# Kernel optimization log

Hardware: AMD Instinct MI355X
Metric: run time of the kernel (lower is better)

The kernel has to match this reference:

```python
import jax, jax.numpy as jnp
import numpy as np

N = 50000       # spatial graph nodes (brain mesh vertices)
K = 1024        # spectral components / spectral-graph nodes
E = 200000      # spatial edges
E_SPEC = 16384  # spectral-graph edges
IN_CH = 3       # vertex coordinates
H = 64          # all hidden_channels forced to 64 by shared LayerNorm(64)
NEG = 0.01      # leaky_relu negative slope (torch default)
EPS = 1e-5      # layernorm eps (torch default)


def _ln(x, g, b):
    mu = jnp.mean(x, -1, keepdims=True)
    var = jnp.mean((x - mu) ** 2, -1, keepdims=True)
    return (x - mu) * jax.lax.rsqrt(var + EPS) * g + b


def _lrelu(x):
    return jnp.where(x >= 0, x, NEG * x)


def _edge_conv(x, ei, W, b, n):
    # PyG EdgeConv: max_j nn(cat([x_i, x_j - x_i])), aggregated at target i = ei[1]
    src, dst = ei[0], ei[1]
    xi = x[dst]
    msg = jnp.concatenate([xi, x[src] - xi], -1) @ W.T + b  # [E, out]
    out = jax.ops.segment_max(msg, dst, num_segments=n)
    return jnp.where(jnp.isfinite(out), out, 0.0)  # zeros for isolated nodes


def _forward(x, u, e, edge_index, spec_edge, p):
    ln = lambda t: _ln(t, p["ln_g"], p["ln_b"])
    s0 = ln(_lrelu(ln(_lrelu(e @ p["se1_w"].T + p["se1_b"])) @ p["se2_w"].T + p["se2_b"]))
    x0 = ln(_lrelu(ln(_lrelu(x @ p["sp1_w"].T + p["sp1_b"])) @ p["sp2_w"].T + p["sp2_b"]))
    s1 = ln(_lrelu(_edge_conv(s0, spec_edge, p["c1_w"], p["c1_b"], K)))
    x1 = ln(_lrelu(_edge_conv(x0, edge_index, p["c5_w"], p["c5_b"], N)))
    s1 = jnp.concatenate([s1, u.T @ x0], 1)   # [K, 128]
    x1 = jnp.concatenate([x1, u @ s0], 1)     # [N, 128]
    s2 = jnp.concatenate([s0, s1], 1)         # [K, 192]
    x2 = jnp.concatenate([x0, x1], 1)         # [N, 192]
    s2 = ln(_lrelu(_edge_conv(s2, spec_edge, p["c2_w"], p["c2_b"], K)))
    x2 = ln(_lrelu(_edge_conv(x2, edge_index, p["c6_w"], p["c6_b"], N)))
    s2 = jnp.concatenate([s2, u.T @ x1], 1)   # [K, 192]
    x2 = jnp.concatenate([x2, u @ s1], 1)     # [N, 192]
    s3 = jnp.concatenate([s0, s1, s2], 1)     # [K, 384]
    x3 = jnp.concatenate([x0, x1, x2], 1)     # [N, 384]
    s3 = ln(_lrelu(_edge_conv(s3, spec_edge, p["c3_w"], p["c3_b"], K)))
    x3 = ln(_lrelu(_edge_conv(x3, edge_index, p["c7_w"], p["c7_b"], N)))
    s3 = jnp.concatenate([s3, u.T @ x2], 1)   # [K, 256]
    x3 = jnp.concatenate([x3, u @ s2], 1)     # [N, 256]
    x4 = jnp.concatenate([x0, x1, x2, x3], 1)  # [N, 640]
    x4 = ln(_lrelu(_edge_conv(x4, edge_index, p["c8_w"], p["c8_b"], N)))
    x4 = jnp.concatenate([x4, u @ s3], 1)      # [N, 320]
    x4 = jnp.concatenate([x0, x1, x2, x3, x4], 1)  # [N, 960]
    out = ln(_lrelu(x4 @ p["d1_w"].T + p["d1_b"]))  # dropout = identity (eval)
    return out @ p["d2_w"].T + p["d2_b"]            # [N, 32]


def setup_inputs() -> dict:
    key = jax.random.key(0)
    ks = iter(jax.random.split(key, 24))
    def w(shape):
        return jax.random.normal(next(ks), shape, jnp.float32) * 0.05
    inp = {
        "x": jax.random.normal(next(ks), (N, IN_CH), jnp.float32),
        "u": jax.random.normal(next(ks), (N, K), jnp.float32) * 0.03,
        "e": jax.random.normal(next(ks), (K, 1), jnp.float32),
        "edge_index": jax.random.randint(next(ks), (2, E), 0, N, jnp.int32),
        "spec_edge": jax.random.randint(next(ks), (2, E_SPEC), 0, K, jnp.int32),
    }
    shapes = {
        "se1_w": (H, 1), "se2_w": (H, H), "sp1_w": (H, IN_CH), "sp2_w": (H, H),
        "c1_w": (H, 2 * 64), "c2_w": (H, 2 * 192), "c3_w": (H, 2 * 384),
        "c5_w": (H, 2 * 64), "c6_w": (H, 2 * 192), "c7_w": (H, 2 * 384),
        "c8_w": (H, 2 * 640), "d1_w": (H, 960), "d2_w": (32, H),
    }
    for name, s in shapes.items():
        inp[name] = w(s)
        inp[name.replace("_w", "_b")] = jnp.zeros((s[0],), jnp.float32)
    inp["ln_g"] = jnp.ones((H,), jnp.float32)
    inp["ln_b"] = jnp.zeros((H,), jnp.float32)
    return inp


def reference(x, u, e, edge_index, spec_edge,
              se1_w, se1_b, se2_w, se2_b, sp1_w, sp1_b, sp2_w, sp2_b,
              c1_w, c1_b, c2_w, c2_b, c3_w, c3_b,
              c5_w, c5_b, c6_w, c6_b, c7_w, c7_b, c8_w, c8_b,
              d1_w, d1_b, d2_w, d2_b, ln_g, ln_b):
    p = dict(locals())
    for k in ("x", "u", "e", "edge_index", "spec_edge"):
        p.pop(k)
    return _forward(x, u, e, edge_index, spec_edge, p)
```

## Files before the change

kernel.cpp:

```cpp
#include <hip/hip_runtime.h>
#include <hip/hip_bf16.h>


typedef __attribute__((ext_vector_type(8))) short bf16x8;
typedef __attribute__((ext_vector_type(4))) float f32x4;

#define DEVFN __device__ __forceinline__

constexpr int NN   = 50000;
constexpr int KKn  = 1024;
constexpr int EEe  = 200000;
constexpr int ESn  = 16384;
constexpr int NPAD = 50016;
constexpr int NKB  = 1563;

DEVFN short f2bf(float v) {
  unsigned b = __float_as_uint(v);
  unsigned r = (b + 0x7FFFu + ((b >> 16) & 1u)) >> 16;
  return (short)r;
}
DEVFN float lrelu(float v) { return v >= 0.f ? v : 0.01f * v; }
DEVFN float wsum64(float v) {
#pragma unroll
  for (int m = 32; m; m >>= 1) v += __shfl_xor(v, m, 64);
  return v;
}
DEVFN float ln64(float v, float g, float b) {
  float mu  = wsum64(v) * 0.015625f;
  float d   = v - mu;
  float var = wsum64(d * d) * 0.015625f;
  return d * rsqrtf(var + 1e-5f) * g + b;
}

__global__ void transpose_u_k(const float* __restrict__ u, short* __restrict__ ub,
                              short* __restrict__ ut) {
  __shared__ float tile[32][33];
  int kt = blockIdx.x, ntile = blockIdx.y;
  int tx = threadIdx.x, ty = threadIdx.y;
#pragma unroll
  for (int r = 0; r < 32; r += 8) {
    int n = ntile * 32 + ty + r;
    int k = kt * 32 + tx;
    float v = 0.f;
    if (n < NN) {
      v = u[(long)n * 1024 + k];
      ub[(long)n * 1024 + k] = f2bf(v);
    }
    tile[ty + r][tx] = v;
  }
  __syncthreads();
#pragma unroll
  for (int r = 0; r < 32; r += 8) {
    int k = kt * 32 + ty + r;
    int n = ntile * 32 + tx;
    ut[(long)k * NPAD + n] = f2bf(tile[tx][ty + r]);
  }
}

__global__ void pack_b_k(const short* __restrict__ src, int lds_, int coloff,
                         int Kred, int kb_total, int C, short* __restrict__ dst) {
  long t = (long)blockIdx.x * 256 + threadIdx.x;
  long total = (long)kb_total * 32 * C;
  if (t >= total) return;
  int k = (int)(t / C);
  int c = (int)(t - (long)k * C);
  short v = (k < Kred) ? src[(long)k * lds_ + coloff + c] : (short)0;
  long pa = (long)(k >> 5) * (32 * C) + ((c >> 4) << 9) + (((k >> 3) & 3) << 7)
          + ((c & 15) << 3) + (k & 7);
  dst[pa] = v;
}

__global__ void pack_wcat_k(const float* __restrict__ W, int F, short* __restrict__ dst) {
  int t = blockIdx.x * 256 + threadIdx.x;
  if (t >= F * 128) return;
  int f = t >> 7, c = t & 127;
  float v = (c < 64) ? (W[c * 2 * F + f] - W[c * 2 * F + F + f])
                     : W[(c - 64) * 2 * F + F + f];
  long pa = (long)(f >> 5) * (32 * 128) + ((c >> 4) << 9) + (((f >> 3) & 3) << 7)
          + ((c & 15) << 3) + (f & 7);
  dst[pa] = f2bf(v);
}

__global__ void pack_d1t_k(const float* __restrict__ W, short* __restrict__ dst) {
  int t = blockIdx.x * 256 + threadIdx.x;
  if (t >= 960 * 64) return;
  int f = t >> 6, c = t & 63;
  float v = W[c * 960 + f];
  long pa = (long)(f >> 5) * (32 * 64) + ((c >> 4) << 9) + (((f >> 3) & 3) << 7)
          + ((c & 15) << 3) + (f & 7);
  dst[pa] = f2bf(v);
}

template <int NT, int EPI>
__launch_bounds__(256)
__global__ void gemm_k(const short* __restrict__ A, int lda,
                       const short* __restrict__ Bp,
                       void* __restrict__ outp, int ldo, int coloff,
                       int M, int kb_total, int kb_chunk) {
  constexpr int C = NT * 16;
  __shared__ short bsm[32 * C];
  const int tid  = threadIdx.x;
  const int lane = tid & 63;
  const int wave = tid >> 6;
  const int mtile = blockIdx.x;
  int kb0 = blockIdx.y * kb_chunk;
  int kb1 = min(kb0 + kb_chunk, kb_total);
  const int row  = mtile * 64 + wave * 16 + (lane & 15);
  const long arow = (long)min(row, M - 1) * lda + ((lane >> 4) * 8);
  f32x4 acc[NT];
#pragma unroll
  for (int t = 0; t < NT; ++t) acc[t] = (f32x4){0.f, 0.f, 0.f, 0.f};

  for (int kb = kb0; kb < kb1; ++kb) {
    const short* bsrc = Bp + (long)kb * (32 * C);
    bf16x8 tmp[NT / 4];
#pragma unroll
    for (int r = 0; r < NT / 4; ++r)
      tmp[r] = *(const bf16x8*)(bsrc + (r * 256 + tid) * 8);
    bf16x8 a = *(const bf16x8*)(A + arow + (long)kb * 32);
    __syncthreads();
#pragma unroll
    for (int r = 0; r < NT / 4; ++r)
      *(bf16x8*)(bsm + (r * 256 + tid) * 8) = tmp[r];
    __syncthreads();
#pragma unroll
    for (int t = 0; t < NT; ++t) {
      bf16x8 b = *(const bf16x8*)(bsm + t * 512 + lane * 8);
      acc[t] = __builtin_amdgcn_mfma_f32_16x16x32_bf16(a, b, acc[t], 0, 0, 0);
    }
  }
  const int cb = lane & 15;
  const int rbase = mtile * 64 + wave * 16 + ((lane >> 4) * 4);
#pragma unroll
  for (int t = 0; t < NT; ++t) {
#pragma unroll
    for (int r = 0; r < 4; ++r) {
      int rr = rbase + r;
      if (rr < M) {
        long idx = (long)rr * ldo + coloff + t * 16 + cb;
        if constexpr (EPI == 0)      ((float*)outp)[idx] = acc[t][r];
        else if constexpr (EPI == 1) ((short*)outp)[idx] = f2bf(acc[t][r]);
        else                          atomicAdd((float*)outp + idx, acc[t][r]);
      }
    }
  }
}

__global__ void mlp_spec_k(const float* __restrict__ e, const float* __restrict__ w1,
                           const float* __restrict__ b1, const float* __restrict__ w2,
                           const float* __restrict__ b2, const float* __restrict__ g,
                           const float* __restrict__ bl, short* __restrict__ feat, int ldf) {
  int t = blockIdx.x * 256 + threadIdx.x;
  int i = t >> 6, lane = t & 63;
  if (i >= KKn) return;
  float ev = e[i];
  float h = lrelu(ev * w1[lane] + b1[lane]);
  h = ln64(h, g[lane], bl[lane]);
  float a = b2[lane];
  for (int j = 0; j < 64; ++j) a += __shfl(h, j, 64) * w2[lane * 64 + j];
  a = lrelu(a); a = ln64(a, g[lane], bl[lane]);
  feat[(long)i * ldf + lane] = f2bf(a);
}

__global__ void mlp_sp_k(const float* __restrict__ x, const float* __restrict__ w1,
                         const float* __restrict__ b1, const float* __restrict__ w2,
                         const float* __restrict__ b2, const float* __restrict__ g,
                         const float* __restrict__ bl, short* __restrict__ feat, int ldf) {
  int t = blockIdx.x * 256 + threadIdx.x;
  int i = t >> 6, lane = t & 63;
  if (i >= NN) return;
  float x0 = x[i * 3 + 0], x1 = x[i * 3 + 1], x2 = x[i * 3 + 2];
  float h = x0 * w1[lane * 3 + 0] + x1 * w1[lane * 3 + 1] + x2 * w1[lane * 3 + 2] + b1[lane];
  h = lrelu(h); h = ln64(h, g[lane], bl[lane]);
  float a = b2[lane];
  for (int j = 0; j < 64; ++j) a += __shfl(h, j, 64) * w2[lane * 64 + j];
  a = lrelu(a); a = ln64(a, g[lane], bl[lane]);
  feat[(long)i * ldf + lane] = f2bf(a);
}

__global__ void edge_max_k(const int* __restrict__ ei, int E, const float* __restrict__ PQ,
                           unsigned* __restrict__ mc) {
  int t = blockIdx.x * 256 + threadIdx.x;
  int e = t >> 6, lane = t & 63;
  if (e >= E) return;
  int src = ei[e], dst = ei[E + e];
  float v = PQ[(long)src * 128 + 64 + lane];
  unsigned b = __float_as_uint(v);
  unsigned code = b ^ ((unsigned)(((int)b) >> 31) | 0x80000000u);
  atomicMax(mc + (long)dst * 64 + lane, code);
}

__global__ void segfin_k(const float* __restrict__ PQ, const unsigned* __restrict__ mc,
                         const float* __restrict__ bias, const float* __restrict__ g,
                         const float* __restrict__ bl, short* __restrict__ feat,
                         int ldf, int coloff, int n) {
  int t = blockIdx.x * 256 + threadIdx.x;
  int i = t >> 6, lane = t & 63;
  if (i >= n) return;
  unsigned code = mc[(long)i * 64 + lane];
  float v = 0.f;
  if (code) {
    unsigned ub = code ^ ((code & 0x80000000u) ? 0x80000000u : 0xFFFFFFFFu);
    v = PQ[(long)i * 128 + lane] + bias[lane] + __uint_as_float(ub);
  }
  v = lrelu(v);
  v = ln64(v, g[lane], bl[lane]);
  feat[(long)i * ldf + coloff + lane] = f2bf(v);
}

__global__ void zconv_k(const float* __restrict__ Z, short* __restrict__ feat,
                        int C, int coloff) {
  int t = blockIdx.x * 256 + threadIdx.x;
  if (t >= KKn * C) return;
  int k = t / C, c = t - k * C;
  feat[(long)k * 640 + coloff + c] = f2bf(Z[t]);
}

__global__ void final_k(const float* __restrict__ H, const float* __restrict__ d1b,
                        const float* __restrict__ d2w, const float* __restrict__ d2b,
                        const float* __restrict__ g, const float* __restrict__ bl,
                        float* __restrict__ out) {
  int t = blockIdx.x * 256 + threadIdx.x;
  int i = t >> 6, lane = t & 63;
  if (i >= NN) return;
  float v = H[(long)i * 64 + lane] + d1b[lane];
  v = lrelu(v);
  v = ln64(v, g[lane], bl[lane]);
  int c = lane & 31;
  int jbase = (lane >> 5) * 32;
  float acc = 0.f;
#pragma unroll
  for (int j = 0; j < 32; ++j)
    acc += __shfl(v, jbase + j, 64) * d2w[c * 64 + jbase + j];
  acc += __shfl_down(acc, 32, 64);
  if (lane < 32) out[(long)i * 32 + c] = acc + d2b[c];
}

extern "C" void kernel_launch(void* const* d_in, const int* in_sizes, int n_in,
                              void* d_out, int out_size, void* d_ws, size_t ws_size,
                              hipStream_t stream) {
  const float* x    = (const float*)d_in[0];
  const float* u    = (const float*)d_in[1];
  const float* e    = (const float*)d_in[2];
  const int*   ei   = (const int*)d_in[3];
  const int*   sei  = (const int*)d_in[4];
  const float* se1w = (const float*)d_in[5];  const float* se1b = (const float*)d_in[6];
  const float* se2w = (const float*)d_in[7];  const float* se2b = (const float*)d_in[8];
  const float* sp1w = (const float*)d_in[9];  const float* sp1b = (const float*)d_in[10];
  const float* sp2w = (const float*)d_in[11]; const float* sp2b = (const float*)d_in[12];
  const float* c1w = (const float*)d_in[13];  const float* c1b = (const float*)d_in[14];
  const float* c2w = (const float*)d_in[15];  const float* c2b = (const float*)d_in[16];
  const float* c3w = (const float*)d_in[17];  const float* c3b = (const float*)d_in[18];
  const float* c5w = (const float*)d_in[19];  const float* c5b = (const float*)d_in[20];
  const float* c6w = (const float*)d_in[21];  const float* c6b = (const float*)d_in[22];
  const float* c7w = (const float*)d_in[23];  const float* c7b = (const float*)d_in[24];
  const float* c8w = (const float*)d_in[25];  const float* c8b = (const float*)d_in[26];
  const float* d1w = (const float*)d_in[27];  const float* d1b = (const float*)d_in[28];
  const float* d2w = (const float*)d_in[29];  const float* d2b = (const float*)d_in[30];
  const float* lng = (const float*)d_in[31];  const float* lnb = (const float*)d_in[32];

  char* ws = (char*)d_ws;
  size_t off = 0;
  auto alloc = [&](size_t bytes) -> void* {
    void* p = ws + off;
    off = (off + bytes + 255) & ~(size_t)255;
    return p;
  };
  short* u_bf  = (short*)alloc((size_t)NN * 1024 * 2);
  short* uT    = (short*)alloc((size_t)KKn * NPAD * 2);
  short* xfeat = (short*)alloc((size_t)NN * 960 * 2);
  short* sfeat = (short*)alloc((size_t)KKn * 640 * 2);
  float* PQx   = (float*)alloc((size_t)NN * 128 * 4);
  float* PQs   = (float*)alloc((size_t)KKn * 128 * 4);
  char* zbase = ws + off;
  unsigned* mx  = (unsigned*)alloc((size_t)NN * 64 * 4);
  unsigned* ms  = (unsigned*)alloc((size_t)KKn * 64 * 4);
  float* Zs0 = (float*)alloc((size_t)KKn * 64 * 4);
  float* Zs1 = (float*)alloc((size_t)KKn * 128 * 4);
  float* Zs2 = (float*)alloc((size_t)KKn * 192 * 4);
  size_t zbytes = (size_t)((ws + off) - zbase);
  short* ypack = (short*)alloc((size_t)KKn * 256 * 2);
  short* zpack = (short*)alloc((size_t)NPAD * 192 * 2);
  short* wc1 = (short*)alloc(64  * 128 * 2);
  short* wc2 = (short*)alloc(192 * 128 * 2);
  short* wc3 = (short*)alloc(384 * 128 * 2);
  short* wc5 = (short*)alloc(64  * 128 * 2);
  short* wc6 = (short*)alloc(192 * 128 * 2);
  short* wc7 = (short*)alloc(384 * 128 * 2);
  short* wc8 = (short*)alloc(640 * 128 * 2);
  short* d1tp = (short*)alloc(960 * 64 * 2);
  float* Hbuf = PQx;

  const size_t MXB = (size_t)NN * 64 * 4;
  const size_t MSB = (size_t)KKn * 64 * 4;

  hipMemsetAsync(zbase, 0, zbytes, stream);
  transpose_u_k<<<dim3(32, NKB), dim3(32, 8), 0, stream>>>(u, u_bf, uT);
  pack_wcat_k<<<32,  256, 0, stream>>>(c1w, 64,  wc1);
  pack_wcat_k<<<96,  256, 0, stream>>>(c2w, 192, wc2);
  pack_wcat_k<<<192, 256, 0, stream>>>(c3w, 384, wc3);
  pack_wcat_k<<<32,  256, 0, stream>>>(c5w, 64,  wc5);
  pack_wcat_k<<<96,  256, 0, stream>>>(c6w, 192, wc6);
  pack_wcat_k<<<192, 256, 0, stream>>>(c7w, 384, wc7);
  pack_wcat_k<<<320, 256, 0, stream>>>(c8w, 640, wc8);
  pack_d1t_k<<<240, 256, 0, stream>>>(d1w, d1tp);
  mlp_spec_k<<<256,   256, 0, stream>>>(e, se1w, se1b, se2w, se2b, lng, lnb, sfeat, 640);
  mlp_sp_k<<<12500,   256, 0, stream>>>(x, sp1w, sp1b, sp2w, sp2b, lng, lnb, xfeat, 960);

  const int GX = (NN + 63) / 64;

  gemm_k<8, 0><<<dim3(GX, 1), 256, 0, stream>>>(xfeat, 960, wc5, PQx, 128, 0, NN, 2, 2);
  gemm_k<8, 0><<<dim3(16, 1), 256, 0, stream>>>(sfeat, 640, wc1, PQs, 128, 0, KKn, 2, 2);
  edge_max_k<<<50000, 256, 0, stream>>>(ei, EEe, PQx, mx);
  edge_max_k<<<4096,  256, 0, stream>>>(sei, ESn, PQs, ms);
  segfin_k<<<12500, 256, 0, stream>>>(PQx, mx, c5b, lng, lnb, xfeat, 960, 64, NN);
  segfin_k<<<256,   256, 0, stream>>>(PQs, ms, c1b, lng, lnb, sfeat, 640, 64, KKn);
  pack_b_k<<<256, 256, 0, stream>>>(sfeat, 640, 0, KKn, 32, 64, ypack);
  gemm_k<4, 1><<<dim3(GX, 1), 256, 0, stream>>>(u_bf, 1024, ypack, xfeat, 960, 128, NN, 32, 32);
  pack_b_k<<<12504, 256, 0, stream>>>(xfeat, 960, 0, NN, NKB, 64, zpack);
  gemm_k<4, 2><<<dim3(16, 16), 256, 0, stream>>>(uT, NPAD, zpack, Zs0, 64, 0, KKn, NKB, 98);
  zconv_k<<<256, 256, 0, stream>>>(Zs0, sfeat, 64, 128);

  hipMemsetAsync(mx, 0, MXB, stream);
  hipMemsetAsync(ms, 0, MSB, stream);
  gemm_k<8, 0><<<dim3(GX, 1), 256, 0, stream>>>(xfeat, 960, wc6, PQx, 128, 0, NN, 6, 6);
  gemm_k<8, 0><<<dim3(16, 1), 256, 0, stream>>>(sfeat, 640, wc2, PQs, 128, 0, KKn, 6, 6);
  edge_max_k<<<50000, 256, 0, stream>>>(ei, EEe, PQx, mx);
  edge_max_k<<<4096,  256, 0, stream>>>(sei, ESn, PQs, ms);
  segfin_k<<<12500, 256, 0, stream>>>(PQx, mx, c6b, lng, lnb, xfeat, 960, 192, NN);
  segfin_k<<<256,   256, 0, stream>>>(PQs, ms, c2b, lng, lnb, sfeat, 640, 192, KKn);
  pack_b_k<<<512, 256, 0, stream>>>(sfeat, 640, 64, KKn, 32, 128, ypack);
  gemm_k<8, 1><<<dim3(GX, 1), 256, 0, stream>>>(u_bf, 1024, ypack, xfeat, 960, 256, NN, 32, 32);
  pack_b_k<<<25008, 256, 0, stream>>>(xfeat, 960, 64, NN, NKB, 128, zpack);
  gemm_k<8, 2><<<dim3(16, 16), 256, 0, stream>>>(uT, NPAD, zpack, Zs1, 128, 0, KKn, NKB, 98);
  zconv_k<<<512, 256, 0, stream>>>(Zs1, sfeat, 128, 256);

  hipMemsetAsync(mx, 0, MXB, stream);
  hipMemsetAsync(ms, 0, MSB, stream);
  gemm_k<8, 0><<<dim3(GX, 1), 256, 0, stream>>>(xfeat, 960, wc7, PQx, 128, 0, NN, 12, 12);
  gemm_k<8, 0><<<dim3(16, 1), 256, 0, stream>>>(sfeat, 640, wc3, PQs, 128, 0, KKn, 12, 12);
  edge_max_k<<<50000, 256, 0, stream>>>(ei, EEe, PQx, mx);
  edge_max_k<<<4096,  256, 0, stream>>>(sei, ESn, PQs, ms);
  segfin_k<<<12500, 256, 0, stream>>>(PQx, mx, c7b, lng, lnb, xfeat, 960, 384, NN);
  segfin_k<<<256,   256, 0, stream>>>(PQs, ms, c3b, lng, lnb, sfeat, 640, 384, KKn);
  pack_b_k<<<768, 256, 0, stream>>>(sfeat, 640, 192, KKn, 32, 192, ypack);
  gemm_k<12, 1><<<dim3(GX, 1), 256, 0, stream>>>(u_bf, 1024, ypack, xfeat, 960, 448, NN, 32, 32);
  pack_b_k<<<37512, 256, 0, stream>>>(xfeat, 960, 192, NN, NKB, 192, zpack);
  gemm_k<12, 2><<<dim3(16, 16), 256, 0, stream>>>(uT, NPAD, zpack, Zs2, 192, 0, KKn, NKB, 98);
  zconv_k<<<768, 256, 0, stream>>>(Zs2, sfeat, 192, 448);

  hipMemsetAsync(mx, 0, MXB, stream);
  gemm_k<8, 0><<<dim3(GX, 1), 256, 0, stream>>>(xfeat, 960, wc8, PQx, 128, 0, NN, 20, 20);
  edge_max_k<<<50000, 256, 0, stream>>>(ei, EEe, PQx, mx);
  segfin_k<<<12500, 256, 0, stream>>>(PQx, mx, c8b, lng, lnb, xfeat, 960, 640, NN);
  pack_b_k<<<1024, 256, 0, stream>>>(sfeat, 640, 384, KKn, 32, 256, ypack);
  gemm_k<16, 1><<<dim3(GX, 1), 256, 0, stream>>>(u_bf, 1024, ypack, xfeat, 960, 704, NN, 32, 32);

  gemm_k<4, 0><<<dim3(GX, 1), 256, 0, stream>>>(xfeat, 960, d1tp, Hbuf, 64, 0, NN, 30, 30);
  final_k<<<12500, 256, 0, stream>>>(Hbuf, d1b, d2w, d2b, lng, lnb, (float*)d_out);

  (void)in_sizes; (void)n_in; (void)out_size; (void)ws_size;
}
```

Baseline: 1.430 ms.

## Merge paired spatial/spectral launches, drop LDS staging in GEMM, widen transpose

Paired spatial and spectral GEMM, edge-max and segment-finalize launches are merged into single kernels that branch on block index, cutting launch count and letting the small spectral work fill gaps. The GEMM no longer stages B through shared memory with two barriers per k-step; each lane reads its pre-packed B fragment straight from global memory, relying on cache reuse across waves. The u transpose now uses 64x64 bf16 tiles with vectorized float4 loads and ushort4 stores, and the padding grows to 50048/1564 to fit the larger tile. Direct global B loads could add cache traffic in place of LDS reads, and the narrow ushort4 transposed stores and LDS bank pattern may not be ideal.

```diff
diff --git a/kernel.cpp b/kernel.cpp
--- a/kernel.cpp
+++ b/kernel.cpp
@@ -11,8 +11,8 @@
 constexpr int KKn  = 1024;
 constexpr int EEe  = 200000;
 constexpr int ESn  = 16384;
-constexpr int NPAD = 50016;
-constexpr int NKB  = 1563;
+constexpr int NPAD = 50048;
+constexpr int NKB  = 1564;
 
 DEVFN short f2bf(float v) {
   unsigned b = __float_as_uint(v);
@@ -34,26 +34,34 @@
 
 __global__ void transpose_u_k(const float* __restrict__ u, short* __restrict__ ub,
                               short* __restrict__ ut) {
-  __shared__ float tile[32][33];
-  int kt = blockIdx.x, ntile = blockIdx.y;
-  int tx = threadIdx.x, ty = threadIdx.y;
-#pragma unroll
-  for (int r = 0; r < 32; r += 8) {
-    int n = ntile * 32 + ty + r;
-    int k = kt * 32 + tx;
-    float v = 0.f;
-    if (n < NN) {
-      v = u[(long)n * 1024 + k];
-      ub[(long)n * 1024 + k] = f2bf(v);
-    }
-    tile[ty + r][tx] = v;
+  __shared__ unsigned short tile[64][66];
+  const int kt  = blockIdx.x;
+  const int nt0 = blockIdx.y;
+  const int tx = threadIdx.x & 15, ty = threadIdx.x >> 4;
+  const int kbase = kt * 64;
+#pragma unroll
+  for (int r = 0; r < 64; r += 16) {
+    int nl = ty + r;
+    int n  = nt0 * 64 + nl;
+    float4 v = {0.f, 0.f, 0.f, 0.f};
+    if (n < NN) v = *(const float4*)(u + (long)n * 1024 + kbase + tx * 4);
+    ushort4 w;
+    w.x = (unsigned short)f2bf(v.x); w.y = (unsigned short)f2bf(v.y);
+    w.z = (unsigned short)f2bf(v.z); w.w = (unsigned short)f2bf(v.w);
+    if (n < NN) *(ushort4*)(ub + (long)n * 1024 + kbase + tx * 4) = w;
+    tile[nl][tx * 4 + 0] = w.x; tile[nl][tx * 4 + 1] = w.y;
+    tile[nl][tx * 4 + 2] = w.z; tile[nl][tx * 4 + 3] = w.w;
   }
   __syncthreads();
 #pragma unroll
-  for (int r = 0; r < 32; r += 8) {
-    int k = kt * 32 + ty + r;
-    int n = ntile * 32 + tx;
-    ut[(long)k * NPAD + n] = f2bf(tile[tx][ty + r]);
+  for (int r = 0; r < 64; r += 16) {
+    int kl = ty + r;
+    int k  = kbase + kl;
+    int n0 = nt0 * 64 + tx * 4;
+    ushort4 w;
+    w.x = tile[tx * 4 + 0][kl]; w.y = tile[tx * 4 + 1][kl];
+    w.z = tile[tx * 4 + 2][kl]; w.w = tile[tx * 4 + 3][kl];
+    *(ushort4*)(ut + (long)k * NPAD + n0) = w;
   }
 }
 
@@ -92,40 +100,25 @@
 }
 
 template <int NT, int EPI>
-__launch_bounds__(256)
-__global__ void gemm_k(const short* __restrict__ A, int lda,
-                       const short* __restrict__ Bp,
-                       void* __restrict__ outp, int ldo, int coloff,
-                       int M, int kb_total, int kb_chunk) {
-  constexpr int C = NT * 16;
-  __shared__ short bsm[32 * C];
-  const int tid  = threadIdx.x;
-  const int lane = tid & 63;
-  const int wave = tid >> 6;
-  const int mtile = blockIdx.x;
-  int kb0 = blockIdx.y * kb_chunk;
-  int kb1 = min(kb0 + kb_chunk, kb_total);
+DEVFN void gemm_body(const short* __restrict__ A, int lda,
+                     const short* __restrict__ Bp,
+                     void* __restrict__ outp, int ldo, int coloff,
+                     int M, int mtile, int kb0, int kb1) {
+  const int lane = threadIdx.x & 63;
+  const int wave = threadIdx.x >> 6;
   const int row  = mtile * 64 + wave * 16 + (lane & 15);
   const long arow = (long)min(row, M - 1) * lda + ((lane >> 4) * 8);
+  const short* bl = Bp + lane * 8;
   f32x4 acc[NT];
 #pragma unroll
   for (int t = 0; t < NT; ++t) acc[t] = (f32x4){0.f, 0.f, 0.f, 0.f};
 
   for (int kb = kb0; kb < kb1; ++kb) {
-    const short* bsrc = Bp + (long)kb * (32 * C);
-    bf16x8 tmp[NT / 4];
-#pragma unroll
-    for (int r = 0; r < NT / 4; ++r)
-      tmp[r] = *(const bf16x8*)(bsrc + (r * 256 + tid) * 8);
     bf16x8 a = *(const bf16x8*)(A + arow + (long)kb * 32);
-    __syncthreads();
-#pragma unroll
-    for (int r = 0; r < NT / 4; ++r)
-      *(bf16x8*)(bsm + (r * 256 + tid) * 8) = tmp[r];
-    __syncthreads();
+    const short* bsrc = bl + (long)kb * (NT * 512);
 #pragma unroll
     for (int t = 0; t < NT; ++t) {
-      bf16x8 b = *(const bf16x8*)(bsm + t * 512 + lane * 8);
+      bf16x8 b = *(const bf16x8*)(bsrc + t * 512);
       acc[t] = __builtin_amdgcn_mfma_f32_16x16x32_bf16(a, b, acc[t], 0, 0, 0);
     }
   }
@@ -146,6 +139,29 @@
   }
 }
 
+template <int NT, int EPI>
+__launch_bounds__(256)
+__global__ void gemm_k(const short* __restrict__ A, int lda,
+                       const short* __restrict__ Bp,
+                       void* __restrict__ outp, int ldo, int coloff,
+                       int M, int kb_total, int kb_chunk) {
+  int kb0 = blockIdx.y * kb_chunk;
+  int kb1 = min(kb0 + kb_chunk, kb_total);
+  gemm_body<NT, EPI>(A, lda, Bp, outp, ldo, coloff, M, blockIdx.x, kb0, kb1);
+}
+
+template <int NT>
+__launch_bounds__(256)
+__global__ void gemmx2_k(const short* __restrict__ A0, int lda0,
+                         const short* __restrict__ B0, float* out0, int M0, int GX0,
+                         const short* __restrict__ A1, int lda1,
+                         const short* __restrict__ B1, float* out1, int M1,
+                         int kb_total) {
+  int b = blockIdx.x;
+  if (b < GX0) gemm_body<NT, 0>(A0, lda0, B0, out0, 128, 0, M0, b, 0, kb_total);
+  else         gemm_body<NT, 0>(A1, lda1, B1, out1, 128, 0, M1, b - GX0, 0, kb_total);
+}
+
 __global__ void mlp_spec_k(const float* __restrict__ e, const float* __restrict__ w1,
                            const float* __restrict__ b1, const float* __restrict__ w2,
                            const float* __restrict__ b2, const float* __restrict__ g,
@@ -178,10 +194,8 @@
   feat[(long)i * ldf + lane] = f2bf(a);
 }
 
-__global__ void edge_max_k(const int* __restrict__ ei, int E, const float* __restrict__ PQ,
-                           unsigned* __restrict__ mc) {
-  int t = blockIdx.x * 256 + threadIdx.x;
-  int e = t >> 6, lane = t & 63;
+DEVFN void edge_max_body(const int* __restrict__ ei, int E, const float* __restrict__ PQ,
+                         unsigned* __restrict__ mc, int e, int lane) {
   if (e >= E) return;
   int src = ei[e], dst = ei[E + e];
   float v = PQ[(long)src * 128 + 64 + lane];
@@ -190,12 +204,25 @@
   atomicMax(mc + (long)dst * 64 + lane, code);
 }
 
-__global__ void segfin_k(const float* __restrict__ PQ, const unsigned* __restrict__ mc,
-                         const float* __restrict__ bias, const float* __restrict__ g,
-                         const float* __restrict__ bl, short* __restrict__ feat,
-                         int ldf, int coloff, int n) {
-  int t = blockIdx.x * 256 + threadIdx.x;
-  int i = t >> 6, lane = t & 63;
+__global__ void edge_max_k(const int* __restrict__ ei, int E, const float* __restrict__ PQ,
+                           unsigned* __restrict__ mc) {
+  int t = blockIdx.x * 256 + threadIdx.x;
+  edge_max_body(ei, E, PQ, mc, t >> 6, t & 63);
+}
+
+__global__ void edge_max2_k(const int* __restrict__ ei0, int E0, const float* __restrict__ PQ0,
+                            unsigned* __restrict__ mc0, int nb0,
+                            const int* __restrict__ ei1, int E1, const float* __restrict__ PQ1,
+                            unsigned* __restrict__ mc1) {
+  int b = blockIdx.x, w = threadIdx.x >> 6, lane = threadIdx.x & 63;
+  if (b < nb0) edge_max_body(ei0, E0, PQ0, mc0, b * 4 + w, lane);
+  else         edge_max_body(ei1, E1, PQ1, mc1, (b - nb0) * 4 + w, lane);
+}
+
+DEVFN void segfin_body(const float* __restrict__ PQ, const unsigned* __restrict__ mc,
+                       const float* __restrict__ bias, const float* __restrict__ g,
+                       const float* __restrict__ bl, short* __restrict__ feat,
+                       int ldf, int coloff, int n, int i, int lane) {
   if (i >= n) return;
   unsigned code = mc[(long)i * 64 + lane];
   float v = 0.f;
@@ -206,6 +233,26 @@
   v = lrelu(v);
   v = ln64(v, g[lane], bl[lane]);
   feat[(long)i * ldf + coloff + lane] = f2bf(v);
+}
+
+__global__ void segfin_k(const float* __restrict__ PQ, const unsigned* __restrict__ mc,
+                         const float* __restrict__ bias, const float* __restrict__ g,
+                         const float* __restrict__ bl, short* __restrict__ feat,
+                         int ldf, int coloff, int n) {
+  int t = blockIdx.x * 256 + threadIdx.x;
+  segfin_body(PQ, mc, bias, g, bl, feat, ldf, coloff, n, t >> 6, t & 63);
+}
+
+__global__ void segfin2_k(const float* __restrict__ PQ0, const unsigned* __restrict__ mc0,
+                          const float* __restrict__ bias0, short* __restrict__ feat0,
+                          int co0, int n0, int nb0,
+                          const float* __restrict__ PQ1, const unsigned* __restrict__ mc1,
+                          const float* __restrict__ bias1, short* __restrict__ feat1,
+                          int co1, int n1,
+                          const float* __restrict__ g, const float* __restrict__ bl) {
+  int b = blockIdx.x, w = threadIdx.x >> 6, lane = threadIdx.x & 63;
+  if (b < nb0) segfin_body(PQ0, mc0, bias0, g, bl, feat0, 960, co0, n0, b * 4 + w, lane);
+  else         segfin_body(PQ1, mc1, bias1, g, bl, feat1, 640, co1, n1, (b - nb0) * 4 + w, lane);
 }
 
 __global__ void zconv_k(const float* __restrict__ Z, short* __restrict__ feat,
@@ -295,7 +342,7 @@
   const size_t MSB = (size_t)KKn * 64 * 4;
 
   hipMemsetAsync(zbase, 0, zbytes, stream);
-  transpose_u_k<<<dim3(32, NKB), dim3(32, 8), 0, stream>>>(u, u_bf, uT);
+  transpose_u_k<<<dim3(16, 782), 256, 0, stream>>>(u, u_bf, uT);
   pack_wcat_k<<<32,  256, 0, stream>>>(c1w, 64,  wc1);
   pack_wcat_k<<<96,  256, 0, stream>>>(c2w, 192, wc2);
   pack_wcat_k<<<192, 256, 0, stream>>>(c3w, 384, wc3);
@@ -309,43 +356,40 @@
 
   const int GX = (NN + 63) / 64;
 
-  gemm_k<8, 0><<<dim3(GX, 1), 256, 0, stream>>>(xfeat, 960, wc5, PQx, 128, 0, NN, 2, 2);
-  gemm_k<8, 0><<<dim3(16, 1), 256, 0, stream>>>(sfeat, 640, wc1, PQs, 128, 0, KKn, 2, 2);
-  edge_max_k<<<50000, 256, 0, stream>>>(ei, EEe, PQx, mx);
-  edge_max_k<<<4096,  256, 0, stream>>>(sei, ESn, PQs, ms);
-  segfin_k<<<12500, 256, 0, stream>>>(PQx, mx, c5b, lng, lnb, xfeat, 960, 64, NN);
-  segfin_k<<<256,   256, 0, stream>>>(PQs, ms, c1b, lng, lnb, sfeat, 640, 64, KKn);
+  gemmx2_k<8><<<GX + 16, 256, 0, stream>>>(xfeat, 960, wc5, PQx, NN, GX,
+                                           sfeat, 640, wc1, PQs, KKn, 2);
+  edge_max2_k<<<50000 + 4096, 256, 0, stream>>>(ei, EEe, PQx, mx, 50000, sei, ESn, PQs, ms);
+  segfin2_k<<<12500 + 256, 256, 0, stream>>>(PQx, mx, c5b, xfeat, 64, NN, 12500,
+                                             PQs, ms, c1b, sfeat, 64, KKn, lng, lnb);
   pack_b_k<<<256, 256, 0, stream>>>(sfeat, 640, 0, KKn, 32, 64, ypack);
   gemm_k<4, 1><<<dim3(GX, 1), 256, 0, stream>>>(u_bf, 1024, ypack, xfeat, 960, 128, NN, 32, 32);
-  pack_b_k<<<12504, 256, 0, stream>>>(xfeat, 960, 0, NN, NKB, 64, zpack);
+  pack_b_k<<<12512, 256, 0, stream>>>(xfeat, 960, 0, NN, NKB, 64, zpack);
   gemm_k<4, 2><<<dim3(16, 16), 256, 0, stream>>>(uT, NPAD, zpack, Zs0, 64, 0, KKn, NKB, 98);
   zconv_k<<<256, 256, 0, stream>>>(Zs0, sfeat, 64, 128);
 
   hipMemsetAsync(mx, 0, MXB, stream);
   hipMemsetAsync(ms, 0, MSB, stream);
-  gemm_k<8, 0><<<dim3(GX, 1), 256, 0, stream>>>(xfeat, 960, wc6, PQx, 128, 0, NN, 6, 6);
-  gemm_k<8, 0><<<dim3(16, 1), 256, 0, stream>>>(sfeat, 640, wc2, PQs, 128, 0, KKn, 6, 6);
-  edge_max_k<<<50000, 256, 0, stream>>>(ei, EEe, PQx, mx);
-  edge_max_k<<<4096,  256, 0, stream>>>(sei, ESn, PQs, ms);
-  segfin_k<<<12500, 256, 0, stream>>>(PQx, mx, c6b, lng, lnb, xfeat, 960, 192, NN);
-  segfin_k<<<256,   256, 0, stream>>>(PQs, ms, c2b, lng, lnb, sfeat, 640, 192, KKn);
+  gemmx2_k<8><<<GX + 16, 256, 0, stream>>>(xfeat, 960, wc6, PQx, NN, GX,
+                                           sfeat, 640, wc2, PQs, KKn, 6);
+  edge_max2_k<<<50000 + 4096, 256, 0, stream>>>(ei, EEe, PQx, mx, 50000, sei, ESn, PQs, ms);
+  segfin2_k<<<12500 + 256, 256, 0, stream>>>(PQx, mx, c6b, xfeat, 192, NN, 12500,
+                                             PQs, ms, c2b, sfeat, 192, KKn, lng, lnb);
   pack_b_k<<<512, 256, 0, stream>>>(sfeat, 640, 64, KKn, 32, 128, ypack);
   gemm_k<8, 1><<<dim3(GX, 1), 256, 0, stream>>>(u_bf, 1024, ypack, xfeat, 960, 256, NN, 32, 32);
-  pack_b_k<<<25008, 256, 0, stream>>>(xfeat, 960, 64, NN, NKB, 128, zpack);
+  pack_b_k<<<25024, 256, 0, stream>>>(xfeat, 960, 64, NN, NKB, 128, zpack);
   gemm_k<8, 2><<<dim3(16, 16), 256, 0, stream>>>(uT, NPAD, zpack, Zs1, 128, 0, KKn, NKB, 98);
   zconv_k<<<512, 256, 0, stream>>>(Zs1, sfeat, 128, 256);
 
   hipMemsetAsync(mx, 0, MXB, stream);
   hipMemsetAsync(ms, 0, MSB, stream);
-  gemm_k<8, 0><<<dim3(GX, 1), 256, 0, stream>>>(xfeat, 960, wc7, PQx, 128, 0, NN, 12, 12);
-  gemm_k<8, 0><<<dim3(16, 1), 256, 0, stream>>>(sfeat, 640, wc3, PQs, 128, 0, KKn, 12, 12);
-  edge_max_k<<<50000, 256, 0, stream>>>(ei, EEe, PQx, mx);
-  edge_max_k<<<4096,  256, 0, stream>>>(sei, ESn, PQs, ms);
-  segfin_k<<<12500, 256, 0, stream>>>(PQx, mx, c7b, lng, lnb, xfeat, 960, 384, NN);
-  segfin_k<<<256,   256, 0, stream>>>(PQs, ms, c3b, lng, lnb, sfeat, 640, 384, KKn);
+  gemmx2_k<8><<<GX + 16, 256, 0, stream>>>(xfeat, 960, wc7, PQx, NN, GX,
+                                           sfeat, 640, wc3, PQs, KKn, 12);
+  edge_max2_k<<<50000 + 4096, 256, 0, stream>>>(ei, EEe, PQx, mx, 50000, sei, ESn, PQs, ms);
+  segfin2_k<<<12500 + 256, 256, 0, stream>>>(PQx, mx, c7b, xfeat, 384, NN, 12500,
+                                             PQs, ms, c3b, sfeat, 384, KKn, lng, lnb);
   pack_b_k<<<768, 256, 0, stream>>>(sfeat, 640, 192, KKn, 32, 192, ypack);
   gemm_k<12, 1><<<dim3(GX, 1), 256, 0, stream>>>(u_bf, 1024, ypack, xfeat, 960, 448, NN, 32, 32);
-  pack_b_k<<<37512, 256, 0, stream>>>(xfeat, 960, 192, NN, NKB, 192, zpack);
+  pack_b_k<<<37536, 256, 0, stream>>>(xfeat, 960, 192, NN, NKB, 192, zpack);
   gemm_k<12, 2><<<dim3(16, 16), 256, 0, stream>>>(uT, NPAD, zpack, Zs2, 192, 0, KKn, NKB, 98);
   zconv_k<<<768, 256, 0, stream>>>(Zs2, sfeat, 192, 448);
 
```

Result: slower. 1.871 ms (+30.8%).
